# Kernel optimization log

Measured on AMD Instinct MI355X. Metric: run time of the kernel, lower is better.

## Reference

```python
import jax, jax.numpy as jnp
import numpy as np

N = 16384      # nodes
E = 65536      # edges
G = 512        # graphs in batch
F_NODE = 9
F_EDGE = 3
H = 64         # hidden_dim
H2 = 32        # hidden_dim // 2
HEADS = 2
DIMS = [(64, 64), (64, 64), (64, 32)]  # (in_dim, out_dim) per NNConv layer
EPS = 1e-5


def setup_inputs() -> dict:
    keys = iter(jax.random.split(jax.random.key(0), 64))

    def nrm(shape, scale=0.05):
        return jax.random.normal(next(keys), shape, jnp.float32) * scale

    inp = {}
    inp["x"] = nrm((N, F_NODE), 1.0)
    src = jax.random.randint(next(keys), (E,), 0, N)
    dst = jax.random.randint(next(keys), (E,), 0, N)
    inp["edge_index"] = jnp.stack([src, dst]).astype(jnp.int32)
    inp["edge_attr"] = nrm((E, F_EDGE), 1.0)
    inp["batch"] = jnp.sort(jax.random.randint(next(keys), (N,), 0, G)).astype(jnp.int32)
    inp["ee_w"] = nrm((F_EDGE, H2)); inp["ee_b"] = nrm((H2,))
    inp["ne_w"] = nrm((F_NODE, H)); inp["ne_b"] = nrm((H,))
    for i, (din, dout) in enumerate(DIMS):
        inp[f"m{i}_w1"] = nrm((H2, H * HEADS)); inp[f"m{i}_b1"] = nrm((H * HEADS,))
        inp[f"m{i}_w2"] = nrm((H * HEADS, din * dout)); inp[f"m{i}_b2"] = nrm((din * dout,))
        inp[f"root{i}"] = nrm((din, dout)); inp[f"cb{i}"] = nrm((dout,))
        inp[f"bn{i}_g"] = jnp.ones((dout,), jnp.float32)
        inp[f"bn{i}_b"] = jnp.zeros((dout,), jnp.float32)
    inp["fc_w"] = nrm((H2, 12)); inp["fc_b"] = nrm((12,))
    return inp


def reference(x, edge_index, edge_attr, batch, ee_w, ee_b, ne_w, ne_b,
              m0_w1, m0_b1, m0_w2, m0_b2, root0, cb0, bn0_g, bn0_b,
              m1_w1, m1_b1, m1_w2, m1_b2, root1, cb1, bn1_g, bn1_b,
              m2_w1, m2_b1, m2_w2, m2_b2, root2, cb2, bn2_g, bn2_b,
              fc_w, fc_b):
    src, dst = edge_index[0], edge_index[1]
    ee = edge_attr @ ee_w + ee_b                 # [E, H2] edge embedding
    h = x @ ne_w + ne_b                          # [N, H] node embedding
    layers = [(m0_w1, m0_b1, m0_w2, m0_b2, root0, cb0, bn0_g, bn0_b),
              (m1_w1, m1_b1, m1_w2, m1_b2, root1, cb1, bn1_g, bn1_b),
              (m2_w1, m2_b1, m2_w2, m2_b2, root2, cb2, bn2_g, bn2_b)]
    deg = jnp.maximum(jax.ops.segment_sum(jnp.ones((E, 1), h.dtype), dst, num_segments=N), 1.0)
    for i, (w1, b1, w2, b2, root, cb, g, bb) in enumerate(layers):
        din, dout = DIMS[i]
        ew = jax.nn.relu(ee @ w1 + b1)           # [E, H*HEADS] edge MLP hidden
        W = (ew @ w2 + b2).reshape(E, din, dout) # per-edge weight matrices
        msg = jnp.einsum('ei,eio->eo', h[src], W)  # gather + per-edge matvec
        aggr = jax.ops.segment_sum(msg, dst, num_segments=N) / deg  # scatter-mean
        h = h @ root + aggr + cb                 # NNConv root weight + bias
        mean = h.mean(0); var = h.var(0)         # BatchNorm1d (batch stats)
        h = jax.nn.relu(g * (h - mean) * jax.lax.rsqrt(var + EPS) + bb)
        # dropout skipped (eval / deterministic reference)
    cnt = jnp.maximum(jax.ops.segment_sum(jnp.ones((N, 1), h.dtype), batch, num_segments=G), 1.0)
    pooled = jax.ops.segment_sum(h, batch, num_segments=G) / cnt  # global_mean_pool
    return jax.nn.sigmoid(pooled @ fc_w + fc_b)
```

## Files before the change

kernel.cpp:

```cpp
#include <hip/hip_runtime.h>
#include <hip/hip_bf16.h>
#include <math.h>

constexpr int NN = 16384;
constexpr int NE = 65536;
constexpr int NG = 512;

typedef __attribute__((ext_vector_type(8)))  short short8;
typedef __attribute__((ext_vector_type(16))) float f32x16;

__device__ __forceinline__ short f2bf(float f) {
    unsigned u = __builtin_bit_cast(unsigned, f);
    return (short)((u + 0x7FFFu + ((u >> 16) & 1u)) >> 16);
}
__device__ __forceinline__ float b2f(unsigned short s) {
    return __builtin_bit_cast(float, (unsigned)s << 16);
}
__device__ __forceinline__ void gload_lds16(const unsigned short* g, unsigned short* l) {
    __builtin_amdgcn_global_load_lds(
        (const __attribute__((address_space(1))) unsigned int*)g,
        (__attribute__((address_space(3))) unsigned int*)l, 16, 0, 0);
}

__device__ __forceinline__ short8 agen(const float* h, float e) {
    unsigned u[4];
#pragma unroll
    for (int q = 0; q < 4; q++) {
        float2 p; p.x = h[2 * q] * e; p.y = h[2 * q + 1] * e;
        __hip_bfloat162 b = __float22bfloat162_rn(p);
        unsigned v; __builtin_memcpy(&v, &b, 4);
        u[q] = v;
    }
    uint4 uv = make_uint4(u[0], u[1], u[2], u[3]);
    return __builtin_bit_cast(short8, uv);
}

__global__ void k_nh(const float* __restrict__ x, const float* __restrict__ w,
                     const float* __restrict__ b, float* __restrict__ h,
                     unsigned short* __restrict__ hbf) {
    int idx = blockIdx.x * 256 + threadIdx.x;
    int n = idx >> 6, o = idx & 63;
    const float* xr = x + n * 9;
    float s = b[o];
#pragma unroll
    for (int a = 0; a < 9; a++) s += xr[a] * w[a * 64 + o];
    h[idx] = s;
    hbf[idx] = (unsigned short)f2bf(s);
}

__global__ void k_deg(const int* __restrict__ ei, float* __restrict__ deg) {
    int e = blockIdx.x * 256 + threadIdx.x;
    atomicAdd(&deg[ei[NE + e]], 1.0f);
}

__global__ __launch_bounds__(256) void k_ewt(const float* __restrict__ ea,
                                             const float* __restrict__ eew,
                                             const float* __restrict__ eeb,
                                             const float* __restrict__ w1,
                                             const float* __restrict__ b1,
                                             unsigned short* __restrict__ ewT) {
    __shared__ float w1s[32 * 128];
    __shared__ float b1s[128];
    __shared__ float eews[96], eebs[32];
    int t = threadIdx.x;
    for (int c = t; c < 4096; c += 256) w1s[c] = w1[c];
    if (t < 128) b1s[t] = b1[t];
    if (t < 96)  eews[t] = eew[t];
    if (t < 32)  eebs[t] = eeb[t];
    __syncthreads();

    int e = blockIdx.x * 64 + (t & 63);
    int w = t >> 6;
    float a0 = ea[e * 3], a1 = ea[e * 3 + 1], a2 = ea[e * 3 + 2];
    float eer[32];
#pragma unroll
    for (int j = 0; j < 32; j++)
        eer[j] = eebs[j] + a0 * eews[j] + a1 * eews[32 + j] + a2 * eews[64 + j];
    float acc[32];
#pragma unroll
    for (int c = 0; c < 32; c++) acc[c] = b1s[w * 32 + c];
    for (int j = 0; j < 32; j++) {
        float ej = eer[j];
#pragma unroll
        for (int c = 0; c < 32; c++) acc[c] += ej * w1s[j * 128 + w * 32 + c];
    }
#pragma unroll
    for (int c = 0; c < 32; c++) {
        float v = fmaxf(acc[c], 0.f);
        ewT[(size_t)(w * 32 + c) * NE + e] = (unsigned short)f2bf(v);
    }
}

template <int DOUT>
__global__ void k_packw2(const float* __restrict__ w2, const float* __restrict__ b2,
                         unsigned short* __restrict__ w2p) {
    constexpr int TILES = DOUT / 32;
    int idx = blockIdx.x * 256 + threadIdx.x;
    int j = idx & 7, l = (idx >> 3) & 63;
    int rest = idx >> 9;
    int tt = rest % TILES;
    int s  = (rest / TILES) & 3;
    int kc = rest / (4 * TILES);
    int i = s * 16 + (l >> 5) * 8 + j;
    int o = tt * 32 + (l & 31);
    float v = (kc < 128) ? w2[(size_t)kc * 64 * DOUT + i * DOUT + o]
                         : (kc == 128 ? b2[i * DOUT + o] : 0.f);
    w2p[idx] = (unsigned short)f2bf(v);
}

template <int DOUT>
__global__ __launch_bounds__(256, 2) void k_msg_mfma(const int* __restrict__ ei,
                                                     const unsigned short* __restrict__ hbf,
                                                     const unsigned short* __restrict__ ewT,
                                                     const unsigned short* __restrict__ w2p,
                                                     float* __restrict__ aggr) {
    constexpr int TILES = DOUT / 32;
    constexpr int SL    = 4 * TILES * 64 * 8;
    constexpr int CH    = 2;
    constexpr int CHSL  = CH * SL;
    constexpr int NCH   = 66;
    __shared__ __align__(16) unsigned short w2s[2 * CHSL];
    __shared__ __align__(16) unsigned short ews[144 * 128];

    int t = threadIdx.x;
    int w = t >> 6, l = t & 63;
    int hi = l >> 5, ln = l & 31;
    int eb = blockIdx.x * 128;
    int e0 = w * 32;

#pragma unroll
    for (int i = 0; i < 9; i++) {
        int idx = i * 256 + t;
        int row = idx >> 4;
        int rowc = row < 128 ? row : 127;
        gload_lds16(ewT + (size_t)rowc * NE + eb + (idx & 15) * 8,
                    ews + idx * 8);
    }
#pragma unroll
    for (int p = 0; p < CHSL / 2048; p++)
        gload_lds16(w2p + p * 2048 + t * 8, w2s + p * 2048 + t * 8);

    float hf[4][8];
    {
        int sidx = ei[eb + e0 + ln];
        const unsigned short* hrow = hbf + (size_t)sidx * 64;
#pragma unroll
        for (int s = 0; s < 4; s++) {
            short8 hv = *(const short8*)(hrow + (s * 2 + hi) * 8);
#pragma unroll
            for (int j = 0; j < 8; j++) hf[s][j] = b2f((unsigned short)hv[j]);
        }
    }

    f32x16 acc[TILES];
#pragma unroll
    for (int tt = 0; tt < TILES; tt++)
#pragma unroll
        for (int r = 0; r < 16; r++) acc[tt][r] = 0.f;

    __syncthreads();

    for (int c = 0; c < NCH; c++) {
        if (c + 1 < NCH) {
            const unsigned short* g = w2p + (size_t)(c + 1) * CHSL;
            unsigned short* ld = w2s + ((c + 1) & 1) * CHSL;
#pragma unroll
            for (int p = 0; p < CHSL / 2048; p++)
                gload_lds16(g + p * 2048 + t * 8, ld + p * 2048 + t * 8);
        }
        const unsigned short* cbuf = w2s + (c & 1) * CHSL;
#pragma unroll
        for (int s2 = 0; s2 < CH; s2++) {
            int kc = c * CH + s2;
            float rv = b2f(ews[kc * 128 + e0 + ln]);
            float ewc = (kc < 128) ? rv : (kc == 128 ? 1.f : 0.f);
            const unsigned short* sbuf = cbuf + s2 * SL;
#pragma unroll
            for (int s = 0; s < 4; s++) {
                short8 a = agen(hf[s], ewc);
#pragma unroll
                for (int tt = 0; tt < TILES; tt++) {
                    short8 b = *(const short8*)(sbuf + ((s * TILES + tt) * 64 + l) * 8);
                    acc[tt] = __builtin_amdgcn_mfma_f32_32x32x16_bf16(a, b, acc[tt], 0, 0, 0);
                }
            }
        }
        __syncthreads();
    }

#pragma unroll
    for (int r = 0; r < 16; r++) {
        int row = (r & 3) + 8 * (r >> 2) + 4 * hi;
        int d = ei[NE + eb + e0 + row];
#pragma unroll
        for (int tt = 0; tt < TILES; tt++)
            atomicAdd(&aggr[(size_t)d * DOUT + tt * 32 + ln], acc[tt][r]);
    }
}

template <int DOUT>
__global__ void k_combine(const float* __restrict__ h, const float* __restrict__ root,
                          const float* __restrict__ aggr, const float* __restrict__ deg,
                          const float* __restrict__ cb, float* __restrict__ htmp) {
    int idx = blockIdx.x * 256 + threadIdx.x;
    int n = idx / DOUT, o = idx % DOUT;
    const float* hr = h + n * 64;
    float s = cb[o] + aggr[idx] / fmaxf(deg[n], 1.f);
#pragma unroll 8
    for (int i = 0; i < 64; i++) s += hr[i] * root[i * DOUT + o];
    htmp[idx] = s;
}

template <int DOUT>
__global__ void k_bnstats(const float* __restrict__ htmp, float* __restrict__ sums) {
    int o = blockIdx.x >> 3, chunk = blockIdx.x & 7, t = threadIdx.x;
    float s = 0.f, q = 0.f;
    int n0 = chunk * (NN / 8);
    for (int n = n0 + t; n < n0 + NN / 8; n += 256) {
        float v = htmp[n * DOUT + o];
        s += v; q += v * v;
    }
    for (int off = 32; off; off >>= 1) { s += __shfl_down(s, off); q += __shfl_down(q, off); }
    __shared__ float ls[4], lq[4];
    int w = t >> 6;
    if ((t & 63) == 0) { ls[w] = s; lq[w] = q; }
    __syncthreads();
    if (t == 0) {
        s = ls[0] + ls[1] + ls[2] + ls[3];
        q = lq[0] + lq[1] + lq[2] + lq[3];
        atomicAdd(&sums[o], s);
        atomicAdd(&sums[DOUT + o], q);
    }
}

template <int DOUT>
__global__ void k_bnfinal(const float* __restrict__ sums, const float* __restrict__ g,
                          const float* __restrict__ bb, float* __restrict__ scale,
                          float* __restrict__ shift) {
    int o = threadIdx.x;
    if (o < DOUT) {
        float mean = sums[o] / NN;
        float var  = sums[DOUT + o] / NN - mean * mean;
        float sc   = g[o] * rsqrtf(var + 1e-5f);
        scale[o] = sc;
        shift[o] = bb[o] - mean * sc;
    }
}

template <int DOUT, bool WB>
__global__ void k_bnapply(const float* __restrict__ htmp, const float* __restrict__ scale,
                          const float* __restrict__ shift, float* __restrict__ hout,
                          unsigned short* __restrict__ hbf) {
    int idx = blockIdx.x * 256 + threadIdx.x;
    int o = idx & (DOUT - 1);
    float v = fmaxf(htmp[idx] * scale[o] + shift[o], 0.f);
    hout[idx] = v;
    if (WB) hbf[idx] = (unsigned short)f2bf(v);
}

__global__ void k_pool(const float* __restrict__ h, const int* __restrict__ batch,
                       float* __restrict__ pool, float* __restrict__ cnt) {
    int idx = blockIdx.x * 256 + threadIdx.x;
    int n = idx >> 5, o = idx & 31;
    int b = batch[n];
    atomicAdd(&pool[b * 32 + o], h[idx]);
    if (o == 0) atomicAdd(&cnt[b], 1.0f);
}

__global__ void k_fc(const float* __restrict__ pool, const float* __restrict__ cnt,
                     const float* __restrict__ w, const float* __restrict__ b,
                     float* __restrict__ out) {
    int idx = blockIdx.x * 256 + threadIdx.x;
    int gI = idx / 12, t = idx % 12;
    float inv = 1.f / fmaxf(cnt[gI], 1.f);
    float s = 0.f;
#pragma unroll 8
    for (int j = 0; j < 32; j++) s += pool[gI * 32 + j] * w[j * 12 + t];
    s = s * inv + b[t];
    out[idx] = 1.f / (1.f + expf(-s));
}

extern "C" void kernel_launch(void* const* d_in, const int* in_sizes, int n_in,
                              void* d_out, int out_size, void* d_ws, size_t ws_size,
                              hipStream_t stream) {
    const float* x   = (const float*)d_in[0];
    const int*   ei  = (const int*)d_in[1];
    const float* ea  = (const float*)d_in[2];
    const int*   bat = (const int*)d_in[3];
    const float* eew = (const float*)d_in[4];
    const float* eeb = (const float*)d_in[5];
    const float* nw  = (const float*)d_in[6];
    const float* nb  = (const float*)d_in[7];
    const float* fcw = (const float*)d_in[32];
    const float* fcb = (const float*)d_in[33];
    float* out = (float*)d_out;

    char* ws = (char*)d_ws;
    unsigned short* ewT = (unsigned short*)(ws + 0);
    unsigned short* w2p = (unsigned short*)(ws + 16777216);
    float* hA    = (float*)(ws + 18874368);
    float* hB    = (float*)(ws + 23068672);
    float* htmp  = (float*)(ws + 27262976);
    float* aggr  = (float*)(ws + 31457280);
    float* sums  = (float*)(ws + 35651584);
    unsigned short* hbf = (unsigned short*)(ws + 35652608);
    float* deg   = (float*)(ws + 37749760);
    float* scale = (float*)(ws + 37815296);
    float* shift = (float*)(ws + 37815552);
    float* pool  = (float*)(ws + 37815808);
    float* cnt   = (float*)(ws + 37881344);

    (void)hipMemsetAsync(deg, 0, NN * 4, stream);
    (void)hipMemsetAsync(pool, 0, NG * 32 * 4 + NG * 4, stream);

    k_nh<<<NN * 64 / 256, 256, 0, stream>>>(x, nw, nb, hA, hbf);
    k_deg<<<NE / 256, 256, 0, stream>>>(ei, deg);

    float* hin = hA;
    float* hout = hB;
    for (int L = 0; L < 3; L++) {
        const float* w1 = (const float*)d_in[8 + 8 * L + 0];
        const float* b1 = (const float*)d_in[8 + 8 * L + 1];
        const float* w2 = (const float*)d_in[8 + 8 * L + 2];
        const float* b2 = (const float*)d_in[8 + 8 * L + 3];
        const float* rt = (const float*)d_in[8 + 8 * L + 4];
        const float* cb = (const float*)d_in[8 + 8 * L + 5];
        const float* bg = (const float*)d_in[8 + 8 * L + 6];
        const float* bb = (const float*)d_in[8 + 8 * L + 7];

        (void)hipMemsetAsync(aggr, 0, NN * 64 * 4 + 1024, stream);

        k_ewt<<<NE / 64, 256, 0, stream>>>(ea, eew, eeb, w1, b1, ewT);

        if (L < 2) {
            k_packw2<64><<<132 * 4096 / 256, 256, 0, stream>>>(w2, b2, w2p);
            k_msg_mfma<64><<<NE / 128, 256, 0, stream>>>(ei, hbf, ewT, w2p, aggr);
            k_combine<64><<<NN * 64 / 256, 256, 0, stream>>>(hin, rt, aggr, deg, cb, htmp);
            k_bnstats<64><<<64 * 8, 256, 0, stream>>>(htmp, sums);
            k_bnfinal<64><<<1, 64, 0, stream>>>(sums, bg, bb, scale, shift);
            k_bnapply<64, true><<<NN * 64 / 256, 256, 0, stream>>>(htmp, scale, shift, hout, hbf);
        } else {
            k_packw2<32><<<132 * 2048 / 256, 256, 0, stream>>>(w2, b2, w2p);
            k_msg_mfma<32><<<NE / 128, 256, 0, stream>>>(ei, hbf, ewT, w2p, aggr);
            k_combine<32><<<NN * 32 / 256, 256, 0, stream>>>(hin, rt, aggr, deg, cb, htmp);
            k_bnstats<32><<<32 * 8, 256, 0, stream>>>(htmp, sums);
            k_bnfinal<32><<<1, 64, 0, stream>>>(sums, bg, bb, scale, shift);
            k_bnapply<32, false><<<NN * 32 / 256, 256, 0, stream>>>(htmp, scale, shift, hout, hbf);
        }
        float* tmp = hin; hin = hout; hout = tmp;
    }
    k_pool<<<NN * 32 / 256, 256, 0, stream>>>(hin, bat, pool, cnt);
    k_fc<<<NG * 12 / 256, 256, 0, stream>>>(pool, cnt, fcw, fcb, out);
}
```

Baseline: 514.4 us.

## Triple-buffer W2 slices with vmcnt waits and fold BN finalize into apply

The message kernel now streams W2 one K-slice at a time through a three-slot LDS ring with two slices in flight. It replaces __syncthreads with an explicit s_waitcnt vmcnt plus s_barrier, so the barrier does not drain every outstanding load. The BN stats kernel is rewritten as a coalesced grid-stride reduction with LDS atomics, and the finalize kernel is merged into the apply kernel so each block recomputes scale and shift. The changes aim to reduce load-latency stalls and launch count, at the cost of more barriers per K step and redundant per-block BN finalize work.

```diff
diff --git a/kernel.cpp b/kernel.cpp
--- a/kernel.cpp
+++ b/kernel.cpp
@@ -116,10 +116,9 @@
                                                      float* __restrict__ aggr) {
     constexpr int TILES = DOUT / 32;
     constexpr int SL    = 4 * TILES * 64 * 8;
-    constexpr int CH    = 2;
-    constexpr int CHSL  = CH * SL;
-    constexpr int NCH   = 66;
-    __shared__ __align__(16) unsigned short w2s[2 * CHSL];
+    constexpr int LPC   = SL / 2048;
+    constexpr int NSL   = 132;
+    __shared__ __align__(16) unsigned short w2s[3 * SL];
     __shared__ __align__(16) unsigned short ews[144 * 128];
 
     int t = threadIdx.x;
@@ -137,8 +136,11 @@
                     ews + idx * 8);
     }
 #pragma unroll
-    for (int p = 0; p < CHSL / 2048; p++)
+    for (int p = 0; p < LPC; p++)
         gload_lds16(w2p + p * 2048 + t * 8, w2s + p * 2048 + t * 8);
+#pragma unroll
+    for (int p = 0; p < LPC; p++)
+        gload_lds16(w2p + SL + p * 2048 + t * 8, w2s + SL + p * 2048 + t * 8);
 
     float hf[4][8];
     {
@@ -158,34 +160,35 @@
 #pragma unroll
         for (int r = 0; r < 16; r++) acc[tt][r] = 0.f;
 
-    __syncthreads();
-
-    for (int c = 0; c < NCH; c++) {
-        if (c + 1 < NCH) {
-            const unsigned short* g = w2p + (size_t)(c + 1) * CHSL;
-            unsigned short* ld = w2s + ((c + 1) & 1) * CHSL;
-#pragma unroll
-            for (int p = 0; p < CHSL / 2048; p++)
+    asm volatile("s_waitcnt vmcnt(%0)" :: "i"(LPC) : "memory");
+    __builtin_amdgcn_s_barrier();
+
+    for (int c = 0; c < NSL; c++) {
+        if (c + 2 < NSL) {
+            const unsigned short* g = w2p + (size_t)(c + 2) * SL;
+            unsigned short* ld = w2s + ((c + 2) % 3) * SL;
+#pragma unroll
+            for (int p = 0; p < LPC; p++)
                 gload_lds16(g + p * 2048 + t * 8, ld + p * 2048 + t * 8);
         }
-        const unsigned short* cbuf = w2s + (c & 1) * CHSL;
-#pragma unroll
-        for (int s2 = 0; s2 < CH; s2++) {
-            int kc = c * CH + s2;
-            float rv = b2f(ews[kc * 128 + e0 + ln]);
-            float ewc = (kc < 128) ? rv : (kc == 128 ? 1.f : 0.f);
-            const unsigned short* sbuf = cbuf + s2 * SL;
-#pragma unroll
-            for (int s = 0; s < 4; s++) {
-                short8 a = agen(hf[s], ewc);
-#pragma unroll
-                for (int tt = 0; tt < TILES; tt++) {
-                    short8 b = *(const short8*)(sbuf + ((s * TILES + tt) * 64 + l) * 8);
-                    acc[tt] = __builtin_amdgcn_mfma_f32_32x32x16_bf16(a, b, acc[tt], 0, 0, 0);
-                }
+        const unsigned short* sbuf = w2s + (c % 3) * SL;
+        float rv = b2f(ews[c * 128 + e0 + ln]);
+        float ewc = (c < 128) ? rv : (c == 128 ? 1.f : 0.f);
+#pragma unroll
+        for (int s = 0; s < 4; s++) {
+            short8 a = agen(hf[s], ewc);
+#pragma unroll
+            for (int tt = 0; tt < TILES; tt++) {
+                short8 b = *(const short8*)(sbuf + ((s * TILES + tt) * 64 + l) * 8);
+                acc[tt] = __builtin_amdgcn_mfma_f32_32x32x16_bf16(a, b, acc[tt], 0, 0, 0);
             }
         }
-        __syncthreads();
+        if (c + 2 < NSL) {
+            asm volatile("s_waitcnt vmcnt(%0)" :: "i"(LPC) : "memory");
+        } else {
+            asm volatile("s_waitcnt vmcnt(0)" ::: "memory");
+        }
+        __builtin_amdgcn_s_barrier();
     }
 
 #pragma unroll
@@ -213,47 +216,42 @@
 
 template <int DOUT>
 __global__ void k_bnstats(const float* __restrict__ htmp, float* __restrict__ sums) {
-    int o = blockIdx.x >> 3, chunk = blockIdx.x & 7, t = threadIdx.x;
+    __shared__ float ls[DOUT], lq[DOUT];
+    int t = threadIdx.x;
+    int o = t & (DOUT - 1);
+    if (t < DOUT) { ls[t] = 0.f; lq[t] = 0.f; }
+    __syncthreads();
     float s = 0.f, q = 0.f;
-    int n0 = chunk * (NN / 8);
-    for (int n = n0 + t; n < n0 + NN / 8; n += 256) {
-        float v = htmp[n * DOUT + o];
+    for (int i = blockIdx.x * 256 + t; i < NN * DOUT; i += 256 * 256) {
+        float v = htmp[i];
         s += v; q += v * v;
     }
-    for (int off = 32; off; off >>= 1) { s += __shfl_down(s, off); q += __shfl_down(q, off); }
-    __shared__ float ls[4], lq[4];
-    int w = t >> 6;
-    if ((t & 63) == 0) { ls[w] = s; lq[w] = q; }
+    atomicAdd(&ls[o], s);
+    atomicAdd(&lq[o], q);
     __syncthreads();
-    if (t == 0) {
-        s = ls[0] + ls[1] + ls[2] + ls[3];
-        q = lq[0] + lq[1] + lq[2] + lq[3];
-        atomicAdd(&sums[o], s);
-        atomicAdd(&sums[DOUT + o], q);
-    }
-}
-
-template <int DOUT>
-__global__ void k_bnfinal(const float* __restrict__ sums, const float* __restrict__ g,
-                          const float* __restrict__ bb, float* __restrict__ scale,
-                          float* __restrict__ shift) {
-    int o = threadIdx.x;
-    if (o < DOUT) {
-        float mean = sums[o] / NN;
-        float var  = sums[DOUT + o] / NN - mean * mean;
-        float sc   = g[o] * rsqrtf(var + 1e-5f);
-        scale[o] = sc;
-        shift[o] = bb[o] - mean * sc;
+    if (t < DOUT) {
+        atomicAdd(&sums[t], ls[t]);
+        atomicAdd(&sums[DOUT + t], lq[t]);
     }
 }
 
 template <int DOUT, bool WB>
-__global__ void k_bnapply(const float* __restrict__ htmp, const float* __restrict__ scale,
-                          const float* __restrict__ shift, float* __restrict__ hout,
-                          unsigned short* __restrict__ hbf) {
-    int idx = blockIdx.x * 256 + threadIdx.x;
+__global__ void k_bnapply(const float* __restrict__ htmp, const float* __restrict__ sums,
+                          const float* __restrict__ g, const float* __restrict__ bb,
+                          float* __restrict__ hout, unsigned short* __restrict__ hbf) {
+    __shared__ float sc[DOUT], sh[DOUT];
+    int t = threadIdx.x;
+    if (t < DOUT) {
+        float mean = sums[t] / NN;
+        float var  = sums[DOUT + t] / NN - mean * mean;
+        float s    = g[t] * rsqrtf(var + 1e-5f);
+        sc[t] = s;
+        sh[t] = bb[t] - mean * s;
+    }
+    __syncthreads();
+    int idx = blockIdx.x * 256 + t;
     int o = idx & (DOUT - 1);
-    float v = fmaxf(htmp[idx] * scale[o] + shift[o], 0.f);
+    float v = fmaxf(htmp[idx] * sc[o] + sh[o], 0.f);
     hout[idx] = v;
     if (WB) hbf[idx] = (unsigned short)f2bf(v);
 }
@@ -305,8 +303,6 @@
     float* sums  = (float*)(ws + 35651584);
     unsigned short* hbf = (unsigned short*)(ws + 35652608);
     float* deg   = (float*)(ws + 37749760);
-    float* scale = (float*)(ws + 37815296);
-    float* shift = (float*)(ws + 37815552);
     float* pool  = (float*)(ws + 37815808);
     float* cnt   = (float*)(ws + 37881344);
 
@@ -336,16 +332,14 @@
             k_packw2<64><<<132 * 4096 / 256, 256, 0, stream>>>(w2, b2, w2p);
             k_msg_mfma<64><<<NE / 128, 256, 0, stream>>>(ei, hbf, ewT, w2p, aggr);
             k_combine<64><<<NN * 64 / 256, 256, 0, stream>>>(hin, rt, aggr, deg, cb, htmp);
-            k_bnstats<64><<<64 * 8, 256, 0, stream>>>(htmp, sums);
-            k_bnfinal<64><<<1, 64, 0, stream>>>(sums, bg, bb, scale, shift);
-            k_bnapply<64, true><<<NN * 64 / 256, 256, 0, stream>>>(htmp, scale, shift, hout, hbf);
+            k_bnstats<64><<<256, 256, 0, stream>>>(htmp, sums);
+            k_bnapply<64, true><<<NN * 64 / 256, 256, 0, stream>>>(htmp, sums, bg, bb, hout, hbf);
         } else {
             k_packw2<32><<<132 * 2048 / 256, 256, 0, stream>>>(w2, b2, w2p);
             k_msg_mfma<32><<<NE / 128, 256, 0, stream>>>(ei, hbf, ewT, w2p, aggr);
             k_combine<32><<<NN * 32 / 256, 256, 0, stream>>>(hin, rt, aggr, deg, cb, htmp);
-            k_bnstats<32><<<32 * 8, 256, 0, stream>>>(htmp, sums);
-            k_bnfinal<32><<<1, 64, 0, stream>>>(sums, bg, bb, scale, shift);
-            k_bnapply<32, false><<<NN * 32 / 256, 256, 0, stream>>>(htmp, scale, shift, hout, hbf);
+            k_bnstats<32><<<256, 256, 0, stream>>>(htmp, sums);
+            k_bnapply<32, false><<<NN * 32 / 256, 256, 0, stream>>>(htmp, sums, bg, bb, hout, hbf);
         }
         float* tmp = hin; hin = hout; hout = tmp;
     }
```

Result: slower. 610.8 us (+18.7%).
